# Optimization experiments

Hardware: AMD Instinct MI355X
Metric: run time of the kernel (lower is better)

The kernel has to match this reference:

```python
import jax, jax.numpy as jnp
import numpy as np

N_NODES = 100000
N_EDGES = 3200000
IN_DIM, HID_DIM, OUT_DIM = 384, 128, 5


def gcn_conv(x, src, dst, W, b, num_nodes):
    # PyG GCNConv: add self-loops, symmetric normalization, linear, aggregate, bias
    h = x @ W  # [N, out]
    ones = jnp.ones(src.shape[0], dtype=h.dtype)
    deg = jax.ops.segment_sum(ones, dst, num_segments=num_nodes)  # includes self-loops
    dinv = jnp.where(deg > 0, jax.lax.rsqrt(deg), 0.0)
    norm = dinv[src] * dinv[dst]  # [E+N]
    msg = h[src] * norm[:, None]
    out = jax.ops.segment_sum(msg, dst, num_segments=num_nodes)
    return out + b


def setup_inputs() -> dict:
    key = jax.random.key(0)
    ks = jax.random.split(key, 8)
    x = jax.random.normal(ks[0], (N_NODES, IN_DIM), dtype=jnp.float32)
    edge_index = jax.random.randint(ks[1], (2, N_EDGES), 0, N_NODES, dtype=jnp.int64)
    # Glorot-ish init for GCN linear weights
    def glorot(k, fi, fo):
        s = jnp.sqrt(6.0 / (fi + fo))
        return jax.random.uniform(k, (fi, fo), jnp.float32, -s, s)
    W1 = glorot(ks[2], IN_DIM, HID_DIM)
    b1 = jnp.zeros((HID_DIM,), jnp.float32)
    W2 = glorot(ks[3], HID_DIM, HID_DIM)
    b2 = jnp.zeros((HID_DIM,), jnp.float32)
    W3 = glorot(ks[4], HID_DIM, OUT_DIM)
    b3 = jnp.zeros((OUT_DIM,), jnp.float32)
    return {"x": x, "edge_index": edge_index, "W1": W1, "b1": b1,
            "W2": W2, "b2": b2, "W3": W3, "b3": b3}


def reference(x, edge_index, W1, b1, W2, b2, W3, b3):
    num_nodes = x.shape[0]
    loops = jnp.arange(num_nodes, dtype=edge_index.dtype)
    src = jnp.concatenate([edge_index[0], loops])
    dst = jnp.concatenate([edge_index[1], loops])
    # layer 1: GCNConv + ReLU (dropout is identity at inference)
    h = jax.nn.relu(gcn_conv(x, src, dst, W1, b1, num_nodes))
    # layer 2
    h = jax.nn.relu(gcn_conv(h, src, dst, W2, b2, num_nodes))
    # final layer: logits, no activation
    return gcn_conv(h, src, dst, W3, b3, num_nodes)
```

## Files before the change

kernel.cpp:

```cpp
#include <hip/hip_runtime.h>
#include <hip/hip_fp16.h>

#define NN 100000
#define NE 3200000
#define SCAN_CHUNK 1024

#define BSH 8
#define BKT_NODES 256
#define NBKT ((NN + BKT_NODES - 1) / BKT_NODES)
#define BIN_BLOCKS 256
#define EPB ((NE + BIN_BLOCKS - 1) / BIN_BLOCKS)
#define GH (NBKT * BIN_BLOCKS)

typedef unsigned int uint;
typedef unsigned short ushort;
typedef __attribute__((ext_vector_type(8))) _Float16 half8;
typedef __attribute__((ext_vector_type(4))) float f32x4;

__device__ inline void gload16(const void* g, void* l) {
    __builtin_amdgcn_global_load_lds(
        (const __attribute__((address_space(1))) void*)g,
        (__attribute__((address_space(3))) void*)l, 16, 0, 0);
}

__device__ inline uint f2h_pair(float a, float b) {
    return (uint)__half_as_ushort(__float2half(a)) |
           ((uint)__half_as_ushort(__float2half(b)) << 16);
}
__device__ inline float h2f_lo(uint u) { return __half2float(__ushort_as_half((ushort)(u & 0xFFFFu))); }
__device__ inline float h2f_hi(uint u) { return __half2float(__ushort_as_half((ushort)(u >> 16))); }
__device__ inline void splitH(float x, ushort& h, ushort& l) {
    __half hh = __float2half(x);
    h = __half_as_ushort(hh);
    l = __half_as_ushort(__float2half(x - __half2float(hh)));
}

__global__ __launch_bounds__(256) void hist_bkt(const int* __restrict__ dst,
                                                int* __restrict__ ghist) {
    __shared__ int h[NBKT];
    int t = threadIdx.x;
    for (int i = t; i < NBKT; i += 256) h[i] = 0;
    __syncthreads();
    int beg = blockIdx.x * EPB;
    int end = beg + EPB; if (end > NE) end = NE;
    for (int e = beg + t; e < end; e += 256)
        atomicAdd(&h[dst[e] >> BSH], 1);
    __syncthreads();
    for (int i = t; i < NBKT; i += 256)
        ghist[i * BIN_BLOCKS + blockIdx.x] = h[i];
}

__global__ __launch_bounds__(256) void scan_p1(const int* __restrict__ cnt,
                                               int* __restrict__ bsum, int N) {
    int t = threadIdx.x;
    int base = blockIdx.x * SCAN_CHUNK + t * 4;
    int s = 0;
#pragma unroll
    for (int q = 0; q < 4; q++) {
        int i = base + q;
        if (i < N) s += cnt[i];
    }
    __shared__ int red[4];
#pragma unroll
    for (int off = 32; off; off >>= 1) s += __shfl_down(s, off, 64);
    if ((t & 63) == 0) red[t >> 6] = s;
    __syncthreads();
    if (t == 0) bsum[blockIdx.x] = red[0] + red[1] + red[2] + red[3];
}

__global__ void scan_p2(int* __restrict__ bsum, int nb) {
    __shared__ int s[128];
    int t = threadIdx.x;
    int v = (t < nb) ? bsum[t] : 0;
    s[t] = v;
    __syncthreads();
    for (int off = 1; off < 128; off <<= 1) {
        int x = s[t];
        int add = (t >= off) ? s[t - off] : 0;
        __syncthreads();
        s[t] = x + add;
        __syncthreads();
    }
    if (t < nb) bsum[t] = s[t] - v;
}

__global__ __launch_bounds__(256) void scan_p3_plain(int* __restrict__ data,
                                                     const int* __restrict__ bsum, int N) {
    __shared__ int ts[256];
    int t = threadIdx.x;
    int base = blockIdx.x * SCAN_CHUNK + t * 4;
    int c[4];
    int s = 0;
#pragma unroll
    for (int q = 0; q < 4; q++) {
        int i = base + q;
        c[q] = (i < N) ? data[i] : 0;
        s += c[q];
    }
    ts[t] = s;
    __syncthreads();
    for (int off = 1; off < 256; off <<= 1) {
        int x = ts[t];
        int add = (t >= off) ? ts[t - off] : 0;
        __syncthreads();
        ts[t] = x + add;
        __syncthreads();
    }
    int run = bsum[blockIdx.x] + ts[t] - s;
#pragma unroll
    for (int q = 0; q < 4; q++) {
        int i = base + q;
        if (i < N) { data[i] = run; run += c[q]; }
    }
}

__global__ __launch_bounds__(256) void bin_edges(const int* __restrict__ src,
                                                 const int* __restrict__ dst,
                                                 const int* __restrict__ ghist,
                                                 uint* __restrict__ binned) {
    __shared__ int cur[NBKT];
    int t = threadIdx.x;
    for (int i = t; i < NBKT; i += 256) cur[i] = ghist[i * BIN_BLOCKS + blockIdx.x];
    __syncthreads();
    int beg = blockIdx.x * EPB;
    int end = beg + EPB; if (end > NE) end = NE;
    for (int e = beg + t; e < end; e += 256) {
        int d = dst[e];
        int b = d >> BSH;
        int p = atomicAdd(&cur[b], 1);
        binned[p] = ((uint)src[e] << BSH) | (uint)(d & (BKT_NODES - 1));
    }
}

__global__ __launch_bounds__(256) void bucket_rowptr(const uint* __restrict__ binned,
                                                     const int* __restrict__ ghist,
                                                     int* __restrict__ rowptr,
                                                     float* __restrict__ dinv) {
    __shared__ int c[BKT_NODES];
    __shared__ int ts[256];
    int t = threadIdx.x;
    int bkt = blockIdx.x;
    c[t] = 0;
    __syncthreads();
    int beg = ghist[bkt * BIN_BLOCKS];
    int end = (bkt == NBKT - 1) ? NE : ghist[(bkt + 1) * BIN_BLOCKS];
    for (int j = beg + t; j < end; j += 256)
        atomicAdd(&c[binned[j] & (BKT_NODES - 1)], 1);
    __syncthreads();
    int ci = c[t];
    ts[t] = ci;
    __syncthreads();
    for (int off = 1; off < 256; off <<= 1) {
        int x = ts[t];
        int add = (t >= off) ? ts[t - off] : 0;
        __syncthreads();
        ts[t] = x + add;
        __syncthreads();
    }
    int node = bkt * BKT_NODES + t;
    if (node < NN) {
        rowptr[node] = beg + ts[t] - ci;
        dinv[node] = 1.0f / sqrtf((float)(ci + 1));
    }
    if (bkt == 0 && t == 0) rowptr[NN] = NE;
}

__global__ __launch_bounds__(256) void csr_fill(const uint* __restrict__ binned,
                                                const int* __restrict__ ghist,
                                                const int* __restrict__ rowptr,
                                                int* __restrict__ col) {
    __shared__ int fill[BKT_NODES];
    int t = threadIdx.x;
    int bkt = blockIdx.x;
    for (int i = t; i < BKT_NODES; i += 256) fill[i] = 0;
    __syncthreads();
    int beg = ghist[bkt * BIN_BLOCKS];
    int end = (bkt == NBKT - 1) ? NE : ghist[(bkt + 1) * BIN_BLOCKS];
    int base = bkt * BKT_NODES;
    for (int j = beg + t; j < end; j += 256) {
        uint r = binned[j];
        int dl = r & (BKT_NODES - 1);
        int p = rowptr[base + dl] + atomicAdd(&fill[dl], 1);
        col[p] = (int)(r >> BSH);
    }
}

template <int K>
__global__ __launch_bounds__(256) void wsplit(const float* __restrict__ W,
                                              ushort* __restrict__ Wth,
                                              ushort* __restrict__ Wtl) {
    __shared__ float tile[32][128];
    int t = threadIdx.x;
    int kb = blockIdx.x;
    {
        int k = t >> 3, cq = t & 7;
#pragma unroll
        for (int q = 0; q < 4; q++) {
            float4 v = *(const float4*)&W[(size_t)(kb * 32 + k) * 128 + cq * 16 + q * 4];
            *(float4*)&tile[k][cq * 16 + q * 4] = v;
        }
    }
    __syncthreads();
    {
        int c = t >> 1, g = t & 1;
        ushort hs[16], ls[16];
#pragma unroll
        for (int i = 0; i < 16; i++) splitH(tile[g * 16 + i][c], hs[i], ls[i]);
        uint h[8], lo[8];
#pragma unroll
        for (int i = 0; i < 8; i++) {
            h[i] = (uint)hs[2 * i] | ((uint)hs[2 * i + 1] << 16);
            lo[i] = (uint)ls[2 * i] | ((uint)ls[2 * i + 1] << 16);
        }
        size_t o = (size_t)c * K + kb * 32 + g * 16;
        *(uint4*)&Wth[o] = make_uint4(h[0], h[1], h[2], h[3]);
        *(uint4*)&Wth[o + 8] = make_uint4(h[4], h[5], h[6], h[7]);
        *(uint4*)&Wtl[o] = make_uint4(lo[0], lo[1], lo[2], lo[3]);
        *(uint4*)&Wtl[o + 8] = make_uint4(lo[4], lo[5], lo[6], lo[7]);
    }
}

template <int K>
__global__ __launch_bounds__(256) void mfma_gemm_f32(const float* __restrict__ X,
                                                     const ushort* __restrict__ Wth,
                                                     const ushort* __restrict__ Wtl,
                                                     const float* __restrict__ dinv,
                                                     uint* __restrict__ Y, int M) {
    __shared__ char smem[32 * 1024];
    char* aF = smem;
    char* bH = smem + 16384;
    char* bL = smem + 24576;
    int tid = threadIdx.x;
    int w = tid >> 6, l = tid & 63;
    int rowBase = blockIdx.x * 128;

    f32x4 acc[2][8];
#pragma unroll
    for (int mf = 0; mf < 2; mf++)
#pragma unroll
        for (int n = 0; n < 8; n++) acc[mf][n] = (f32x4){0.f, 0.f, 0.f, 0.f};

    int fc = l & 15, fkg = l >> 4;

    for (int kt = 0; kt < K; kt += 32) {
#pragma unroll
        for (int i = 0; i < 4; i++) {
            int cb = (i * 4 + w) * 64;
            int c = cb + l;
            int kq = c >> 7, row = c & 127;
            int gr = rowBase + row;
            if (gr >= M) gr = 0;
            gload16(&X[(size_t)gr * K + kt + kq * 4], aF + cb * 16);
        }
#pragma unroll
        for (int i = 0; i < 2; i++) {
            int cb = (i * 4 + w) * 64;
            int c = cb + l;
            int kg = c >> 7, colb = c & 127;
            size_t go = (size_t)colb * K + kt + kg * 8;
            gload16(&Wth[go], bH + cb * 16);
            gload16(&Wtl[go], bL + cb * 16);
        }
        __syncthreads();

#pragma unroll
        for (int mf = 0; mf < 2; mf++) {
            int mrow = (2 * w + mf) * 16 + fc;
            f32x4 p0 = *(const f32x4*)(aF + (2 * fkg) * 2048 + mrow * 16);
            f32x4 p1 = *(const f32x4*)(aF + (2 * fkg + 1) * 2048 + mrow * 16);
            half8 av;
            av[0] = (_Float16)p0[0]; av[1] = (_Float16)p0[1];
            av[2] = (_Float16)p0[2]; av[3] = (_Float16)p0[3];
            av[4] = (_Float16)p1[0]; av[5] = (_Float16)p1[1];
            av[6] = (_Float16)p1[2]; av[7] = (_Float16)p1[3];
#pragma unroll
            for (int n = 0; n < 8; n++) {
                int boff = fkg * 2048 + (16 * n + fc) * 16;
                half8 bh = *(const half8*)(bH + boff);
                half8 bl = *(const half8*)(bL + boff);
                acc[mf][n] = __builtin_amdgcn_mfma_f32_16x16x32_f16(av, bh, acc[mf][n], 0, 0, 0);
                acc[mf][n] = __builtin_amdgcn_mfma_f32_16x16x32_f16(av, bl, acc[mf][n], 0, 0, 0);
            }
        }
        __syncthreads();
    }

#pragma unroll
    for (int mf = 0; mf < 2; mf++) {
        float dscale[4];
#pragma unroll
        for (int r = 0; r < 4; r++) {
            int row = rowBase + (2 * w + mf) * 16 + fkg * 4 + r;
            dscale[r] = (row < M) ? dinv[row] : 0.f;
        }
#pragma unroll
        for (int n = 0; n < 8; n++) {
#pragma unroll
            for (int r = 0; r < 4; r++) {
                float val = acc[mf][n][r] * dscale[r];
                float p = __shfl_xor(val, 1, 64);
                int row = rowBase + (2 * w + mf) * 16 + fkg * 4 + r;
                if (!(l & 1) && row < M)
                    Y[(size_t)row * 64 + 8 * n + (fc >> 1)] = f2h_pair(val, p);
            }
        }
    }
}

__global__ __launch_bounds__(256) void mfma_gemm_f16(const ushort* __restrict__ Xh,
                                                     const ushort* __restrict__ Wth,
                                                     const ushort* __restrict__ Wtl,
                                                     const float* __restrict__ dinv,
                                                     uint* __restrict__ Y, int M) {
    __shared__ char smem[24 * 1024];
    char* aP = smem;
    char* bH = smem + 8192;
    char* bL = smem + 16384;
    int tid = threadIdx.x;
    int w = tid >> 6, l = tid & 63;
    int rowBase = blockIdx.x * 128;

    f32x4 acc[2][8];
#pragma unroll
    for (int mf = 0; mf < 2; mf++)
#pragma unroll
        for (int n = 0; n < 8; n++) acc[mf][n] = (f32x4){0.f, 0.f, 0.f, 0.f};

    int fc = l & 15, fkg = l >> 4;
    int aoff0 = fkg * 2048 + ((2 * w + 0) * 16 + fc) * 16;
    int aoff1 = fkg * 2048 + ((2 * w + 1) * 16 + fc) * 16;

    for (int kt = 0; kt < 128; kt += 32) {
#pragma unroll
        for (int i = 0; i < 2; i++) {
            int cb = (i * 4 + w) * 64;
            int c = cb + l;
            int kg = c >> 7, idx = c & 127;
            gload16(&Xh[(size_t)(rowBase + idx) * 128 + kt + kg * 8], aP + cb * 16);
            gload16(&Wth[(size_t)idx * 128 + kt + kg * 8], bH + cb * 16);
            gload16(&Wtl[(size_t)idx * 128 + kt + kg * 8], bL + cb * 16);
        }
        __syncthreads();
        half8 av0 = *(const half8*)(aP + aoff0);
        half8 av1 = *(const half8*)(aP + aoff1);
#pragma unroll
        for (int n = 0; n < 8; n++) {
            int boff = fkg * 2048 + (16 * n + fc) * 16;
            half8 bh = *(const half8*)(bH + boff);
            half8 bl = *(const half8*)(bL + boff);
            acc[0][n] = __builtin_amdgcn_mfma_f32_16x16x32_f16(av0, bh, acc[0][n], 0, 0, 0);
            acc[0][n] = __builtin_amdgcn_mfma_f32_16x16x32_f16(av0, bl, acc[0][n], 0, 0, 0);
            acc[1][n] = __builtin_amdgcn_mfma_f32_16x16x32_f16(av1, bh, acc[1][n], 0, 0, 0);
            acc[1][n] = __builtin_amdgcn_mfma_f32_16x16x32_f16(av1, bl, acc[1][n], 0, 0, 0);
        }
        __syncthreads();
    }

#pragma unroll
    for (int mf = 0; mf < 2; mf++) {
        float dscale[4];
#pragma unroll
        for (int r = 0; r < 4; r++) {
            int row = rowBase + (2 * w + mf) * 16 + fkg * 4 + r;
            dscale[r] = (row < M) ? dinv[row] : 0.f;
        }
#pragma unroll
        for (int n = 0; n < 8; n++) {
#pragma unroll
            for (int r = 0; r < 4; r++) {
                float val = acc[mf][n][r] * dscale[r];
                float p = __shfl_xor(val, 1, 64);
                int row = rowBase + (2 * w + mf) * 16 + fkg * 4 + r;
                if (!(l & 1) && row < M)
                    Y[(size_t)row * 64 + 8 * n + (fc >> 1)] = f2h_pair(val, p);
            }
        }
    }
}

__global__ __launch_bounds__(256) void gemm_n5h(const uint4* __restrict__ Xh,
                                                const float* __restrict__ W,
                                                const float* __restrict__ dinv,
                                                uint4* __restrict__ hc, int M) {
    __shared__ float wl[640];
    int t = threadIdx.x;
    for (int i = t; i < 640; i += 256) wl[i] = W[i];
    __syncthreads();
    int row = blockIdx.x * 256 + t;
    if (row >= M) return;
    float acc0 = 0.f, acc1 = 0.f, acc2 = 0.f, acc3 = 0.f, acc4 = 0.f;
#pragma unroll
    for (int kq = 0; kq < 16; kq++) {
        uint4 v = Xh[(size_t)row * 16 + kq];
        uint uu[4] = {v.x, v.y, v.z, v.w};
#pragma unroll
        for (int e = 0; e < 4; e++) {
            float x0 = h2f_lo(uu[e]);
            float x1 = h2f_hi(uu[e]);
            int k = kq * 8 + e * 2;
            acc0 = fmaf(x0, wl[k * 5 + 0], acc0); acc0 = fmaf(x1, wl[k * 5 + 5], acc0);
            acc1 = fmaf(x0, wl[k * 5 + 1], acc1); acc1 = fmaf(x1, wl[k * 5 + 6], acc1);
            acc2 = fmaf(x0, wl[k * 5 + 2], acc2); acc2 = fmaf(x1, wl[k * 5 + 7], acc2);
            acc3 = fmaf(x0, wl[k * 5 + 3], acc3); acc3 = fmaf(x1, wl[k * 5 + 8], acc3);
            acc4 = fmaf(x0, wl[k * 5 + 4], acc4); acc4 = fmaf(x1, wl[k * 5 + 9], acc4);
        }
    }
    float di = dinv[row];
    hc[row] = make_uint4(f2h_pair(acc0 * di, acc1 * di),
                         f2h_pair(acc2 * di, acc3 * di),
                         f2h_pair(acc4 * di, 0.f), 0u);
}

#define ACC8H(v)                              \
    a0 += h2f_lo(v.x); a1 += h2f_hi(v.x);     \
    a2 += h2f_lo(v.y); a3 += h2f_hi(v.y);     \
    a4 += h2f_lo(v.z); a5 += h2f_hi(v.z);     \
    a6 += h2f_lo(v.w); a7 += h2f_hi(v.w);

__global__ __launch_bounds__(256) void agg128_v3(const uint4* __restrict__ hb4,
                                                 const int* __restrict__ rowptr,
                                                 const int* __restrict__ col,
                                                 const float* __restrict__ dinv,
                                                 const float* __restrict__ bias,
                                                 uint4* __restrict__ out, int N, int do_relu) {
    int wave = threadIdx.x >> 6;
    int lane = threadIdx.x & 63;
    int node = blockIdx.x * 4 + wave;
    if (node >= N) return;
    int g = lane >> 4;
    int q = lane & 15;
    int beg = rowptr[node], end = rowptr[node + 1];
    float a0 = 0.f, a1 = 0.f, a2 = 0.f, a3 = 0.f, a4 = 0.f, a5 = 0.f, a6 = 0.f, a7 = 0.f;

    int j = beg;
    for (; j + 16 <= end; j += 16) {
        int s0 = col[j + g];
        int s1 = col[j + 4 + g];
        int s2 = col[j + 8 + g];
        int s3 = col[j + 12 + g];
        uint4 v0 = hb4[(size_t)s0 * 16 + q];
        uint4 v1 = hb4[(size_t)s1 * 16 + q];
        uint4 v2 = hb4[(size_t)s2 * 16 + q];
        uint4 v3 = hb4[(size_t)s3 * 16 + q];
        ACC8H(v0); ACC8H(v1); ACC8H(v2); ACC8H(v3);
    }
    if (j + 8 <= end) {
        int s0 = col[j + g];
        int s1 = col[j + 4 + g];
        uint4 v0 = hb4[(size_t)s0 * 16 + q];
        uint4 v1 = hb4[(size_t)s1 * 16 + q];
        ACC8H(v0); ACC8H(v1);
        j += 8;
    }
    if (j < end) {
        int jj0 = j + g, jj1 = j + 4 + g;
        bool p0 = jj0 < end, p1 = jj1 < end;
        int s0 = p0 ? col[jj0] : node;
        int s1 = p1 ? col[jj1] : node;
        uint4 v0 = hb4[(size_t)s0 * 16 + q];
        uint4 v1 = hb4[(size_t)s1 * 16 + q];
        if (!p0) v0 = make_uint4(0u, 0u, 0u, 0u);
        if (!p1) v1 = make_uint4(0u, 0u, 0u, 0u);
        ACC8H(v0); ACC8H(v1);
    }
#pragma unroll
    for (int off = 16; off <= 32; off <<= 1) {
        a0 += __shfl_xor(a0, off, 64);
        a1 += __shfl_xor(a1, off, 64);
        a2 += __shfl_xor(a2, off, 64);
        a3 += __shfl_xor(a3, off, 64);
        a4 += __shfl_xor(a4, off, 64);
        a5 += __shfl_xor(a5, off, 64);
        a6 += __shfl_xor(a6, off, 64);
        a7 += __shfl_xor(a7, off, 64);
    }
    if (g == 0) {
        uint4 vs = hb4[(size_t)node * 16 + q];
        ACC8H(vs);
        float di = dinv[node];
        const float4* bias4 = (const float4*)bias;
        float4 bb0 = bias4[q * 2], bb1 = bias4[q * 2 + 1];
        float o0 = a0 * di + bb0.x, o1 = a1 * di + bb0.y;
        float o2 = a2 * di + bb0.z, o3 = a3 * di + bb0.w;
        float o4 = a4 * di + bb1.x, o5 = a5 * di + bb1.y;
        float o6 = a6 * di + bb1.z, o7 = a7 * di + bb1.w;
        if (do_relu) {
            o0 = fmaxf(o0, 0.f); o1 = fmaxf(o1, 0.f);
            o2 = fmaxf(o2, 0.f); o3 = fmaxf(o3, 0.f);
            o4 = fmaxf(o4, 0.f); o5 = fmaxf(o5, 0.f);
            o6 = fmaxf(o6, 0.f); o7 = fmaxf(o7, 0.f);
        }
        out[(size_t)node * 16 + q] =
            make_uint4(f2h_pair(o0, o1), f2h_pair(o2, o3), f2h_pair(o4, o5), f2h_pair(o6, o7));
    }
}

__global__ void agg5_v2(const uint4* __restrict__ hc, const int* __restrict__ rowptr,
                        const int* __restrict__ col, const float* __restrict__ dinv,
                        const float* __restrict__ b3, float* __restrict__ out, int N) {
    int node = blockIdx.x * 256 + threadIdx.x;
    if (node >= N) return;
    float a0 = 0.f, a1 = 0.f, a2 = 0.f, a3 = 0.f, a4 = 0.f;
    int beg = rowptr[node], end = rowptr[node + 1];
#pragma unroll 2
    for (int j = beg; j < end; ++j) {
        uint4 v = hc[col[j]];
        a0 += h2f_lo(v.x); a1 += h2f_hi(v.x);
        a2 += h2f_lo(v.y); a3 += h2f_hi(v.y);
        a4 += h2f_lo(v.z);
    }
    uint4 vs = hc[node];
    a0 += h2f_lo(vs.x); a1 += h2f_hi(vs.x);
    a2 += h2f_lo(vs.y); a3 += h2f_hi(vs.y);
    a4 += h2f_lo(vs.z);
    float di = dinv[node];
    out[node * 5 + 0] = a0 * di + b3[0];
    out[node * 5 + 1] = a1 * di + b3[1];
    out[node * 5 + 2] = a2 * di + b3[2];
    out[node * 5 + 3] = a3 * di + b3[3];
    out[node * 5 + 4] = a4 * di + b3[4];
}

static inline size_t align512(size_t x) { return (x + 511) & ~(size_t)511; }

extern "C" void kernel_launch(void* const* d_in, const int* in_sizes, int n_in,
                              void* d_out, int out_size, void* d_ws, size_t ws_size,
                              hipStream_t stream) {
    const float* x  = (const float*)d_in[0];
    const int* ei   = (const int*)d_in[1];
    const float* W1 = (const float*)d_in[2];
    const float* b1 = (const float*)d_in[3];
    const float* W2 = (const float*)d_in[4];
    const float* b2 = (const float*)d_in[5];
    const float* W3 = (const float*)d_in[6];
    const float* b3 = (const float*)d_in[7];
    const int* src = ei;
    const int* dst = ei + NE;

    char* ws = (char*)d_ws;
    size_t off = 0;
    int* rowptr = (int*)(ws + off);     off += align512((size_t)(NN + 1) * 4);
    float* dinv = (float*)(ws + off);   off += align512((size_t)NN * 4);
    int* bsum = (int*)(ws + off);       off += align512((size_t)128 * 4);
    int* ghist = (int*)(ws + off);      off += align512((size_t)GH * 4);
    ushort* wt1h = (ushort*)(ws + off); off += align512((size_t)128 * 384 * 2);
    ushort* wt1l = (ushort*)(ws + off); off += align512((size_t)128 * 384 * 2);
    ushort* wt2h = (ushort*)(ws + off); off += align512((size_t)128 * 128 * 2);
    ushort* wt2l = (ushort*)(ws + off); off += align512((size_t)128 * 128 * 2);
    int* col = (int*)(ws + off);        off += align512((size_t)NE * 4);
    uint* hb = (uint*)(ws + off);       off += align512((size_t)NN * 64 * 4);
    char* bufF = (char*)(ws + off);     off += align512((size_t)NN * 128 * 4);
    uint4* hc = (uint4*)(ws + off);     off += align512((size_t)NN * 16);
    uint* binned = (uint*)bufF;
    (void)ws_size;

    wsplit<384><<<12, 256, 0, stream>>>(W1, wt1h, wt1l);
    wsplit<128><<<4, 256, 0, stream>>>(W2, wt2h, wt2l);

    hist_bkt<<<BIN_BLOCKS, 256, 0, stream>>>(dst, ghist);
    {
        int nb = (GH + SCAN_CHUNK - 1) / SCAN_CHUNK;
        scan_p1<<<nb, 256, 0, stream>>>(ghist, bsum, GH);
        scan_p2<<<1, 128, 0, stream>>>(bsum, nb);
        scan_p3_plain<<<nb, 256, 0, stream>>>(ghist, bsum, GH);
    }
    bin_edges<<<BIN_BLOCKS, 256, 0, stream>>>(src, dst, ghist, binned);
    bucket_rowptr<<<NBKT, 256, 0, stream>>>(binned, ghist, rowptr, dinv);
    csr_fill<<<NBKT, 256, 0, stream>>>(binned, ghist, rowptr, col);

    int gemm_blocks = (NN + 127) / 128;
    mfma_gemm_f32<384><<<gemm_blocks, 256, 0, stream>>>(x, wt1h, wt1l, dinv, hb, NN);
    agg128_v3<<<(NN + 3) / 4, 256, 0, stream>>>((const uint4*)hb, rowptr, col, dinv, b1,
                                                (uint4*)bufF, NN, 1);
    mfma_gemm_f16<<<gemm_blocks, 256, 0, stream>>>((const ushort*)bufF, wt2h, wt2l, dinv, hb, NN);
    agg128_v3<<<(NN + 3) / 4, 256, 0, stream>>>((const uint4*)hb, rowptr, col, dinv, b2,
                                                (uint4*)bufF, NN, 1);
    gemm_n5h<<<(NN + 255) / 256, 256, 0, stream>>>((const uint4*)bufF, W3, dinv, hc, NN);
    agg5_v2<<<(NN + 255) / 256, 256, 0, stream>>>(hc, rowptr, col, dinv, b3, (float*)d_out, NN);
}
```

Before: 461.2 us.

## Fuse bucket rowptr and CSR fill; prefetch A tile to registers as fp16

Merges the bucket_rowptr and csr_fill kernels into one kernel. Each bucket's binned records are cached in LDS so the second pass reads them from shared memory instead of global memory, and the separate rowptr read goes away. The first-layer GEMM now loads X rows into registers one k-tile ahead, converts them to fp16 and writes them to LDS, instead of async-copying fp32 tiles to LDS. This shrinks LDS use and overlaps the global loads with the MFMA work. The costs are higher register pressure and a larger LDS footprint in the CSR kernel, which may reduce occupancy.

```diff
diff --git a/kernel.cpp b/kernel.cpp
--- a/kernel.cpp
+++ b/kernel.cpp
@@ -11,6 +11,7 @@
 #define BIN_BLOCKS 256
 #define EPB ((NE + BIN_BLOCKS - 1) / BIN_BLOCKS)
 #define GH (NBKT * BIN_BLOCKS)
+#define REC_CAP 9216
 
 typedef unsigned int uint;
 typedef unsigned short ushort;
@@ -132,20 +133,32 @@
     }
 }
 
-__global__ __launch_bounds__(256) void bucket_rowptr(const uint* __restrict__ binned,
-                                                     const int* __restrict__ ghist,
-                                                     int* __restrict__ rowptr,
-                                                     float* __restrict__ dinv) {
+__global__ __launch_bounds__(256) void bucket_csr(const uint* __restrict__ binned,
+                                                  const int* __restrict__ ghist,
+                                                  int* __restrict__ rowptr,
+                                                  float* __restrict__ dinv,
+                                                  int* __restrict__ col) {
+    __shared__ uint rec[REC_CAP];
     __shared__ int c[BKT_NODES];
     __shared__ int ts[256];
     int t = threadIdx.x;
     int bkt = blockIdx.x;
-    c[t] = 0;
-    __syncthreads();
     int beg = ghist[bkt * BIN_BLOCKS];
     int end = (bkt == NBKT - 1) ? NE : ghist[(bkt + 1) * BIN_BLOCKS];
-    for (int j = beg + t; j < end; j += 256)
-        atomicAdd(&c[binned[j] & (BKT_NODES - 1)], 1);
+    int n = end - beg;
+    bool fits = (n <= REC_CAP);
+    c[t] = 0;
+    __syncthreads();
+    if (fits) {
+        for (int i = t; i < n; i += 256) {
+            uint r = binned[beg + i];
+            rec[i] = r;
+            atomicAdd(&c[r & (BKT_NODES - 1)], 1);
+        }
+    } else {
+        for (int j = beg + t; j < end; j += 256)
+            atomicAdd(&c[binned[j] & (BKT_NODES - 1)], 1);
+    }
     __syncthreads();
     int ci = c[t];
     ts[t] = ci;
@@ -157,31 +170,28 @@
         ts[t] = x + add;
         __syncthreads();
     }
+    int excl = ts[t] - ci;
     int node = bkt * BKT_NODES + t;
     if (node < NN) {
-        rowptr[node] = beg + ts[t] - ci;
+        rowptr[node] = beg + excl;
         dinv[node] = 1.0f / sqrtf((float)(ci + 1));
     }
     if (bkt == 0 && t == 0) rowptr[NN] = NE;
-}
-
-__global__ __launch_bounds__(256) void csr_fill(const uint* __restrict__ binned,
-                                                const int* __restrict__ ghist,
-                                                const int* __restrict__ rowptr,
-                                                int* __restrict__ col) {
-    __shared__ int fill[BKT_NODES];
-    int t = threadIdx.x;
-    int bkt = blockIdx.x;
-    for (int i = t; i < BKT_NODES; i += 256) fill[i] = 0;
-    __syncthreads();
-    int beg = ghist[bkt * BIN_BLOCKS];
-    int end = (bkt == NBKT - 1) ? NE : ghist[(bkt + 1) * BIN_BLOCKS];
-    int base = bkt * BKT_NODES;
-    for (int j = beg + t; j < end; j += 256) {
-        uint r = binned[j];
-        int dl = r & (BKT_NODES - 1);
-        int p = rowptr[base + dl] + atomicAdd(&fill[dl], 1);
-        col[p] = (int)(r >> BSH);
+    __syncthreads();
+    c[t] = beg + excl;
+    __syncthreads();
+    if (fits) {
+        for (int i = t; i < n; i += 256) {
+            uint r = rec[i];
+            int p = atomicAdd(&c[r & (BKT_NODES - 1)], 1);
+            col[p] = (int)(r >> BSH);
+        }
+    } else {
+        for (int j = beg + t; j < end; j += 256) {
+            uint r = binned[j];
+            int p = atomicAdd(&c[r & (BKT_NODES - 1)], 1);
+            col[p] = (int)(r >> BSH);
+        }
     }
 }
 
@@ -226,10 +236,10 @@
                                                      const ushort* __restrict__ Wtl,
                                                      const float* __restrict__ dinv,
                                                      uint* __restrict__ Y, int M) {
-    __shared__ char smem[32 * 1024];
-    char* aF = smem;
-    char* bH = smem + 16384;
-    char* bL = smem + 24576;
+    __shared__ char smem[24 * 1024];
+    char* aP = smem;
+    char* bH = smem + 8192;
+    char* bL = smem + 16384;
     int tid = threadIdx.x;
     int w = tid >> 6, l = tid & 63;
     int rowBase = blockIdx.x * 128;
@@ -240,18 +250,25 @@
 #pragma unroll
         for (int n = 0; n < 8; n++) acc[mf][n] = (f32x4){0.f, 0.f, 0.f, 0.f};
 
+    int sRow = tid >> 1, sKp = tid & 1;
+    int gRow = rowBase + sRow;
+    bool rowOK = gRow < M;
+    size_t aBase = (size_t)(rowOK ? gRow : 0) * K + sKp * 16;
+
+    float4 a0, a1, a2, a3;
+    a0 = a1 = a2 = a3 = make_float4(0.f, 0.f, 0.f, 0.f);
+    if (rowOK) {
+        a0 = *(const float4*)&X[aBase];
+        a1 = *(const float4*)&X[aBase + 4];
+        a2 = *(const float4*)&X[aBase + 8];
+        a3 = *(const float4*)&X[aBase + 12];
+    }
+
     int fc = l & 15, fkg = l >> 4;
+    int aoff0 = fkg * 2048 + ((2 * w + 0) * 16 + fc) * 16;
+    int aoff1 = fkg * 2048 + ((2 * w + 1) * 16 + fc) * 16;
 
     for (int kt = 0; kt < K; kt += 32) {
-#pragma unroll
-        for (int i = 0; i < 4; i++) {
-            int cb = (i * 4 + w) * 64;
-            int c = cb + l;
-            int kq = c >> 7, row = c & 127;
-            int gr = rowBase + row;
-            if (gr >= M) gr = 0;
-            gload16(&X[(size_t)gr * K + kt + kq * 4], aF + cb * 16);
-        }
 #pragma unroll
         for (int i = 0; i < 2; i++) {
             int cb = (i * 4 + w) * 64;
@@ -261,26 +278,36 @@
             gload16(&Wth[go], bH + cb * 16);
             gload16(&Wtl[go], bL + cb * 16);
         }
-        __syncthreads();
-
-#pragma unroll
-        for (int mf = 0; mf < 2; mf++) {
-            int mrow = (2 * w + mf) * 16 + fc;
-            f32x4 p0 = *(const f32x4*)(aF + (2 * fkg) * 2048 + mrow * 16);
-            f32x4 p1 = *(const f32x4*)(aF + (2 * fkg + 1) * 2048 + mrow * 16);
-            half8 av;
-            av[0] = (_Float16)p0[0]; av[1] = (_Float16)p0[1];
-            av[2] = (_Float16)p0[2]; av[3] = (_Float16)p0[3];
-            av[4] = (_Float16)p1[0]; av[5] = (_Float16)p1[1];
-            av[6] = (_Float16)p1[2]; av[7] = (_Float16)p1[3];
-#pragma unroll
-            for (int n = 0; n < 8; n++) {
-                int boff = fkg * 2048 + (16 * n + fc) * 16;
-                half8 bh = *(const half8*)(bH + boff);
-                half8 bl = *(const half8*)(bL + boff);
-                acc[mf][n] = __builtin_amdgcn_mfma_f32_16x16x32_f16(av, bh, acc[mf][n], 0, 0, 0);
-                acc[mf][n] = __builtin_amdgcn_mfma_f32_16x16x32_f16(av, bl, acc[mf][n], 0, 0, 0);
-            }
+        {
+            float v[16] = {a0.x, a0.y, a0.z, a0.w, a1.x, a1.y, a1.z, a1.w,
+                           a2.x, a2.y, a2.z, a2.w, a3.x, a3.y, a3.z, a3.w};
+            uint hh[8];
+#pragma unroll
+            for (int i = 0; i < 8; i++) hh[i] = f2h_pair(v[2 * i], v[2 * i + 1]);
+            *(uint4*)(aP + (2 * sKp) * 2048 + sRow * 16) = make_uint4(hh[0], hh[1], hh[2], hh[3]);
+            *(uint4*)(aP + (2 * sKp + 1) * 2048 + sRow * 16) = make_uint4(hh[4], hh[5], hh[6], hh[7]);
+        }
+        __syncthreads();
+
+        if (kt + 32 < K && rowOK) {
+            size_t nb = aBase + kt + 32;
+            a0 = *(const float4*)&X[nb];
+            a1 = *(const float4*)&X[nb + 4];
+            a2 = *(const float4*)&X[nb + 8];
+            a3 = *(const float4*)&X[nb + 12];
+        }
+
+        half8 av0 = *(const half8*)(aP + aoff0);
+        half8 av1 = *(const half8*)(aP + aoff1);
+#pragma unroll
+        for (int n = 0; n < 8; n++) {
+            int boff = fkg * 2048 + (16 * n + fc) * 16;
+            half8 bh = *(const half8*)(bH + boff);
+            half8 bl = *(const half8*)(bL + boff);
+            acc[0][n] = __builtin_amdgcn_mfma_f32_16x16x32_f16(av0, bh, acc[0][n], 0, 0, 0);
+            acc[0][n] = __builtin_amdgcn_mfma_f32_16x16x32_f16(av0, bl, acc[0][n], 0, 0, 0);
+            acc[1][n] = __builtin_amdgcn_mfma_f32_16x16x32_f16(av1, bh, acc[1][n], 0, 0, 0);
+            acc[1][n] = __builtin_amdgcn_mfma_f32_16x16x32_f16(av1, bl, acc[1][n], 0, 0, 0);
         }
         __syncthreads();
     }
@@ -565,8 +592,7 @@
         scan_p3_plain<<<nb, 256, 0, stream>>>(ghist, bsum, GH);
     }
     bin_edges<<<BIN_BLOCKS, 256, 0, stream>>>(src, dst, ghist, binned);
-    bucket_rowptr<<<NBKT, 256, 0, stream>>>(binned, ghist, rowptr, dinv);
-    csr_fill<<<NBKT, 256, 0, stream>>>(binned, ghist, rowptr, col);
+    bucket_csr<<<NBKT, 256, 0, stream>>>(binned, ghist, rowptr, dinv, col);
 
     int gemm_blocks = (NN + 127) / 128;
     mfma_gemm_f32<384><<<gemm_blocks, 256, 0, stream>>>(x, wt1h, wt1l, dinv, hb, NN);
```

Result: faster. 439.6 us, median of 3 (-4.7%).
